# Kernel optimization log

Hardware: AMD Instinct MI355X
Metric: run time of the kernel (lower is better)

Reference implementation:

```python
import jax, jax.numpy as jnp
import numpy as np

EMBED = 2048
HEADS = 16
DFF = 4 * EMBED
EPS = 1e-5


def layernorm(x, g, b):
    mu = jnp.mean(x, axis=-1, keepdims=True)
    var = jnp.var(x, axis=-1, keepdims=True)
    return (x - mu) * jax.lax.rsqrt(var + EPS) * g + b


def setup_inputs() -> dict:
    key = jax.random.key(0)
    ks = jax.random.split(key, 16)
    s = 1.0 / np.sqrt(EMBED)
    sf = 1.0 / np.sqrt(DFF)
    return {
        "x": jax.random.normal(ks[0], (2, 2048, EMBED), jnp.float32),
        "Wq": jax.random.normal(ks[1], (EMBED, EMBED), jnp.float32) * s,
        "bq": jnp.zeros((EMBED,), jnp.float32),
        "Wk": jax.random.normal(ks[2], (EMBED, EMBED), jnp.float32) * s,
        "bk": jnp.zeros((EMBED,), jnp.float32),
        "Wv": jax.random.normal(ks[3], (EMBED, EMBED), jnp.float32) * s,
        "bv": jnp.zeros((EMBED,), jnp.float32),
        "Wo": jax.random.normal(ks[4], (EMBED, EMBED), jnp.float32) * s,
        "bo": jnp.zeros((EMBED,), jnp.float32),
        "g1": jnp.ones((EMBED,), jnp.float32),
        "b1": jnp.zeros((EMBED,), jnp.float32),
        "g2": jnp.ones((EMBED,), jnp.float32),
        "b2": jnp.zeros((EMBED,), jnp.float32),
        "W1": jax.random.normal(ks[5], (EMBED, DFF), jnp.float32) * s,
        "bf1": jnp.zeros((DFF,), jnp.float32),
        "W2": jax.random.normal(ks[6], (DFF, EMBED), jnp.float32) * sf,
        "bf2": jnp.zeros((EMBED,), jnp.float32),
    }


def reference(x, Wq, bq, Wk, bk, Wv, bv, Wo, bo, g1, b1, g2, b2, W1, bf1, W2, bf2):
    B, N, C = x.shape
    H = HEADS
    hd = C // H
    # QKV projections -> [B, H, N, hd]
    def split_heads(t):
        return t.reshape(B, N, H, hd).transpose(0, 2, 1, 3)
    q = split_heads(x @ Wq + bq)
    k = split_heads(x @ Wk + bk)
    v = split_heads(x @ Wv + bv)
    # scores [B, H, N, N]
    attn = jnp.einsum('bhqd,bhkd->bhqk', q, k) / np.sqrt(hd)
    attn = jax.nn.softmax(attn, axis=-1)
    out = jnp.einsum('bhqk,bhkd->bhqd', attn, v)
    out = out.transpose(0, 2, 1, 3).reshape(B, N, C)
    out = out @ Wo + bo
    h = layernorm(x + out, g1, b1)
    ff = jax.nn.gelu(h @ W1 + bf1, approximate=False) @ W2 + bf2
    return layernorm(h + ff, g2, b2)
```

## Files before the change

### kernel.cpp

```cpp
#include <hip/hip_runtime.h>
#include <math.h>

#define EMBED 2048
#define DFF   8192
#define TOK   4096
#define SEQ   2048
#define HEADS 16
#define HD    128
#define LDQ   6144

typedef __attribute__((ext_vector_type(8))) short short8;
typedef __attribute__((ext_vector_type(4))) float f32x4;

__device__ __forceinline__ unsigned short f2bf(float f) {
    unsigned int u = __float_as_uint(f);
    return (unsigned short)((u + 0x7FFFu + ((u >> 16) & 1u)) >> 16);
}
__device__ __forceinline__ float bf2f(unsigned short s) {
    return __uint_as_float(((unsigned int)s) << 16);
}

__device__ __forceinline__ void async16(const void* g, void* l) {
    __builtin_amdgcn_global_load_lds((const __attribute__((address_space(1))) void*)g,
                                     (__attribute__((address_space(3))) void*)l, 16, 0, 0);
}

template<int MODE>
__global__ __launch_bounds__(256, 2)
void gemm_bf16(const unsigned short* __restrict__ A, const unsigned short* __restrict__ B,
               const float* __restrict__ bias, const void* __restrict__ resid,
               unsigned short* __restrict__ C, int M, int N, int K, int lda)
{
    __shared__ unsigned short As[128*32];
    __shared__ unsigned short Bs[128*32];
    const int t = threadIdx.x;
    const int w = t >> 6, l = t & 63;
    const int quad = l >> 4, m16 = l & 15;
    const long bm = (long)blockIdx.y * 128, bn = (long)blockIdx.x * 128;
    const int wr = (w >> 1)*64, wc = (w & 1)*64;

    f32x4 acc[4][4] = {};

    const int srow = w*16 + (l >> 2);
    const int sslot = l & 3;

    for (int k0 = 0; k0 < K; k0 += 32) {
        __syncthreads();
#pragma unroll
        for (int u = 0; u < 2; ++u) {
            const int row = u*64 + srow;
            const int c = sslot ^ ((row >> 1) & 3);
            async16(A + (size_t)(bm + row)*lda + k0 + c*8, As + u*2048 + w*512);
            async16(B + (size_t)(bn + row)*K   + k0 + c*8, Bs + u*2048 + w*512);
        }
        __syncthreads();
        short8 af[4], bf[4];
#pragma unroll
        for (int s = 0; s < 4; ++s) {
            const int ra = wr + s*16 + m16;
            const int sla = quad ^ ((ra >> 1) & 3);
            af[s] = *(const short8*)&As[ra*32 + sla*8];
            const int rb = wc + s*16 + m16;
            const int slb = quad ^ ((rb >> 1) & 3);
            bf[s] = *(const short8*)&Bs[rb*32 + slb*8];
        }
#pragma unroll
        for (int ms = 0; ms < 4; ++ms)
#pragma unroll
            for (int ns = 0; ns < 4; ++ns)
                acc[ms][ns] = __builtin_amdgcn_mfma_f32_16x16x32_bf16(af[ms], bf[ns], acc[ms][ns], 0, 0, 0);
    }

#pragma unroll
    for (int ns = 0; ns < 4; ++ns) {
        const long gc = bn + wc + ns*16 + m16;
        const float bcol = bias[gc];
#pragma unroll
        for (int ms = 0; ms < 4; ++ms) {
#pragma unroll
            for (int r = 0; r < 4; ++r) {
                const long gr = bm + wr + ms*16 + quad*4 + r;
                float v = acc[ms][ns][r] + bcol;
                if (MODE == 1) v += ((const float*)resid)[gr*N + gc];
                if (MODE == 3) v += bf2f(((const unsigned short*)resid)[gr*N + gc]);
                if (MODE == 2) v = 0.5f*v*(1.0f + erff(v*0.70710678118654752f));
                C[gr*N + gc] = f2bf(v);
            }
        }
    }
}

__global__ __launch_bounds__(256, 2)
void attn_flash(unsigned short* __restrict__ qkv)
{
    __shared__ unsigned short Qs[64*128];
    __shared__ unsigned short Ks[64*128];
    __shared__ unsigned short Vt[128*72];
    __shared__ unsigned short Ps[4*16*72];

    const int t = threadIdx.x;
    const int w = t >> 6, l = t & 63;
    const int quad = l >> 4, m16 = l & 15;

    const int qt = blockIdx.x & 31;
    const int bh = blockIdx.x >> 5;
    const int b = bh >> 4, h = bh & 15;

    const long rowq = (long)b*SEQ + qt*64;
    const int qc = h*HD;
    const int kc = EMBED + h*HD;
    const int vc = 2*EMBED + h*HD;

    {
        const int rbase = w*4 + (l >> 4);
        const int slot = l & 15;
#pragma unroll
        for (int u = 0; u < 4; ++u) {
            const int row = u*16 + rbase;
            const int c = slot ^ ((row >> 1) & 7);
            async16(qkv + (rowq + row)*LDQ + qc + c*8, Qs + u*2048 + w*512);
        }
    }
    __syncthreads();

    short8 af[4];
#pragma unroll
    for (int ks = 0; ks < 4; ++ks) {
        const int row = w*16 + m16;
        const int sl = (4*ks + quad) ^ ((row >> 1) & 7);
        af[ks] = *(const short8*)&Qs[row*128 + sl*8];
    }

    f32x4 O[8] = {};
    float mrun[4] = {-1e30f,-1e30f,-1e30f,-1e30f};
    float lrun[4] = {0.f,0.f,0.f,0.f};
    unsigned short* Pw = Ps + w*16*72;

    for (int kt = 0; kt < SEQ/64; ++kt) {
        const long rowkv = (long)b*SEQ + kt*64;
        __syncthreads();
        {
            const int rbase = w*4 + (l >> 4);
            const int slot = l & 15;
#pragma unroll
            for (int u = 0; u < 4; ++u) {
                const int row = u*16 + rbase;
                const int c = slot ^ ((row >> 1) & 7);
                async16(qkv + (rowkv + row)*LDQ + kc + c*8, Ks + u*2048 + w*512);
            }
        }
        {
            const int slot = t & 15;
#pragma unroll
            for (int u = 0; u < 2; ++u) {
                const int rp = u*16 + (t >> 4);
                const short8 va = *(const short8*)(qkv + (rowkv + 2*rp    )*LDQ + vc + slot*8);
                const short8 vb = *(const short8*)(qkv + (rowkv + 2*rp + 1)*LDQ + vc + slot*8);
#pragma unroll
                for (int i = 0; i < 8; ++i) {
                    const int d = slot*8 + i;
                    const int col = (2*rp) ^ (((d >> 5) & 3) << 3);
                    unsigned int pv = (unsigned int)(unsigned short)va[i] |
                                      ((unsigned int)(unsigned short)vb[i] << 16);
                    *(unsigned int*)&Vt[d*72 + col] = pv;
                }
            }
        }
        __syncthreads();

        f32x4 S[4];
#pragma unroll
        for (int ns = 0; ns < 4; ++ns) {
            f32x4 a = {0.f,0.f,0.f,0.f};
            const int row = ns*16 + m16;
            const int swr = (row >> 1) & 7;
#pragma unroll
            for (int ks = 0; ks < 4; ++ks) {
                const int sl = (4*ks + quad) ^ swr;
                const short8 bf = *(const short8*)&Ks[row*128 + sl*8];
                a = __builtin_amdgcn_mfma_f32_16x16x32_bf16(af[ks], bf, a, 0, 0, 0);
            }
#pragma unroll
            for (int r = 0; r < 4; ++r) a[r] *= 0.08838834764831845f;
            S[ns] = a;
        }

        float al[4], rs[4];
#pragma unroll
        for (int r = 0; r < 4; ++r) {
            float tm = fmaxf(fmaxf(S[0][r], S[1][r]), fmaxf(S[2][r], S[3][r]));
            tm = fmaxf(tm, __shfl_xor(tm, 1));
            tm = fmaxf(tm, __shfl_xor(tm, 2));
            tm = fmaxf(tm, __shfl_xor(tm, 4));
            tm = fmaxf(tm, __shfl_xor(tm, 8));
            const float mn = fmaxf(mrun[r], tm);
            al[r] = __expf(mrun[r] - mn);
            mrun[r] = mn;
            rs[r] = 0.f;
        }
#pragma unroll
        for (int ns = 0; ns < 4; ++ns)
#pragma unroll
            for (int r = 0; r < 4; ++r) {
                const float p = __expf(S[ns][r] - mrun[r]);
                rs[r] += p;
                Pw[(quad*4 + r)*72 + ns*16 + m16] = f2bf(p);
            }
#pragma unroll
        for (int r = 0; r < 4; ++r) {
            rs[r] += __shfl_xor(rs[r], 1);
            rs[r] += __shfl_xor(rs[r], 2);
            rs[r] += __shfl_xor(rs[r], 4);
            rs[r] += __shfl_xor(rs[r], 8);
            lrun[r] = lrun[r]*al[r] + rs[r];
        }
#pragma unroll
        for (int i = 0; i < 8; ++i)
#pragma unroll
            for (int r = 0; r < 4; ++r) O[i][r] *= al[r];

#pragma unroll
        for (int ks2 = 0; ks2 < 2; ++ks2) {
            const short8 ap = *(const short8*)&Pw[m16*72 + ks2*32 + quad*8];
#pragma unroll
            for (int ds = 0; ds < 8; ++ds) {
                const int d = ds*16 + m16;
                const int jcol = (ks2*32 + quad*8) ^ (((d >> 5) & 3) << 3);
                const short8 bv = *(const short8*)&Vt[d*72 + jcol];
                O[ds] = __builtin_amdgcn_mfma_f32_16x16x32_bf16(ap, bv, O[ds], 0, 0, 0);
            }
        }
    }

    float inv[4];
#pragma unroll
    for (int r = 0; r < 4; ++r) inv[r] = 1.0f / lrun[r];
#pragma unroll
    for (int ds = 0; ds < 8; ++ds)
#pragma unroll
        for (int r = 0; r < 4; ++r) {
            const long row = rowq + w*16 + quad*4 + r;
            qkv[row*LDQ + qc + ds*16 + m16] = f2bf(O[ds][r] * inv[r]);
        }
}

template<int OUTF32>
__global__ __launch_bounds__(256)
void ln_bf16(const unsigned short* __restrict__ X, const float* __restrict__ g,
             const float* __restrict__ be, void* __restrict__ Y)
{
    __shared__ float r1[256], r2[256];
    const int t = threadIdx.x;
    const long row = blockIdx.x;
    const unsigned short* x = X + row*EMBED;
    float v[8];
    const short8 xv = *(const short8*)(x + t*8);
    float s = 0.f, s2 = 0.f;
#pragma unroll
    for (int i = 0; i < 8; ++i) {
        v[i] = bf2f((unsigned short)xv[i]);
        s += v[i]; s2 += v[i]*v[i];
    }
    r1[t] = s; r2[t] = s2;
    __syncthreads();
    for (int k = 128; k > 0; k >>= 1) {
        if (t < k) { r1[t] += r1[t+k]; r2[t] += r2[t+k]; }
        __syncthreads();
    }
    const float mu = r1[0] * (1.0f/EMBED);
    const float var = r2[0] * (1.0f/EMBED) - mu*mu;
    const float rstd = rsqrtf(var + 1e-5f);
    if (OUTF32) {
        float* y = (float*)Y + row*EMBED + t*8;
#pragma unroll
        for (int i = 0; i < 8; ++i) y[i] = (v[i]-mu)*rstd*g[t*8+i] + be[t*8+i];
    } else {
        unsigned short* y = (unsigned short*)Y + row*EMBED;
        short8 o;
#pragma unroll
        for (int i = 0; i < 8; ++i) o[i] = (short)f2bf((v[i]-mu)*rstd*g[t*8+i] + be[t*8+i]);
        *(short8*)(y + t*8) = o;
    }
}

__global__ __launch_bounds__(256)
void cvt_transpose(const float* __restrict__ W, unsigned short* __restrict__ Wt, int K, int N)
{
    __shared__ unsigned short T[32][33];
    const int t = threadIdx.x;
    const long n0 = (long)blockIdx.x*32, k0 = (long)blockIdx.y*32;
    {
        const int r = t >> 3, c = (t & 7)*4;
        const float4 vv = *(const float4*)&W[(k0 + r)*N + n0 + c];
        T[r][c+0] = f2bf(vv.x); T[r][c+1] = f2bf(vv.y);
        T[r][c+2] = f2bf(vv.z); T[r][c+3] = f2bf(vv.w);
    }
    __syncthreads();
    const int rn = t >> 3, kk = (t & 7)*4;
    unsigned int p0 = (unsigned int)T[kk+0][rn] | ((unsigned int)T[kk+1][rn] << 16);
    unsigned int p1 = (unsigned int)T[kk+2][rn] | ((unsigned int)T[kk+3][rn] << 16);
    unsigned int* dst = (unsigned int*)&Wt[(n0 + rn)*K + k0 + kk];
    dst[0] = p0; dst[1] = p1;
}

__global__ __launch_bounds__(256)
void cvt_f32_bf16(const float* __restrict__ X, unsigned short* __restrict__ Y, long n)
{
    const long i = ((long)blockIdx.x*256 + threadIdx.x)*8;
    if (i >= n) return;
    const float4 a = *(const float4*)&X[i];
    const float4 b = *(const float4*)&X[i+4];
    short8 o;
    o[0]=(short)f2bf(a.x); o[1]=(short)f2bf(a.y); o[2]=(short)f2bf(a.z); o[3]=(short)f2bf(a.w);
    o[4]=(short)f2bf(b.x); o[5]=(short)f2bf(b.y); o[6]=(short)f2bf(b.z); o[7]=(short)f2bf(b.w);
    *(short8*)&Y[i] = o;
}

__global__ __launch_bounds__(256)
void concat_bias(const float* __restrict__ bq, const float* __restrict__ bk,
                 const float* __restrict__ bv, float* __restrict__ out)
{
    const int i = blockIdx.x*256 + threadIdx.x;
    if (i < 2048) out[i] = bq[i];
    else if (i < 4096) out[i] = bk[i-2048];
    else if (i < 6144) out[i] = bv[i-4096];
}

extern "C" void kernel_launch(void* const* d_in, const int* in_sizes, int n_in,
                              void* d_out, int out_size, void* d_ws, size_t ws_size,
                              hipStream_t stream)
{
    const float* x   = (const float*)d_in[0];
    const float* Wq  = (const float*)d_in[1];
    const float* bq  = (const float*)d_in[2];
    const float* Wk  = (const float*)d_in[3];
    const float* bk  = (const float*)d_in[4];
    const float* Wv  = (const float*)d_in[5];
    const float* bv  = (const float*)d_in[6];
    const float* Wo  = (const float*)d_in[7];
    const float* bo  = (const float*)d_in[8];
    const float* g1  = (const float*)d_in[9];
    const float* b1  = (const float*)d_in[10];
    const float* g2v = (const float*)d_in[11];
    const float* b2v = (const float*)d_in[12];
    const float* W1  = (const float*)d_in[13];
    const float* bf1 = (const float*)d_in[14];
    const float* W2  = (const float*)d_in[15];
    const float* bf2 = (const float*)d_in[16];
    float* out = (float*)d_out;

    char* ws = (char*)d_ws;
    unsigned short* Wqkvt = (unsigned short*)(ws + 0);
    unsigned short* Wot   = (unsigned short*)(ws + 25165824);
    unsigned short* W1t   = (unsigned short*)(ws + 33554432);
    unsigned short* W2t   = (unsigned short*)(ws + 67108864);
    float*          bqkv  = (float*)         (ws + 100663296);
    char* arenaA = ws + 100687872;
    unsigned short* xb   = (unsigned short*)(arenaA);
    unsigned short* qkv  = (unsigned short*)(arenaA + 16777216);
    unsigned short* res1 = (unsigned short*)(arenaA);
    unsigned short* ff   = (unsigned short*)(arenaA);
    unsigned short* hb   = (unsigned short*)(ws + 167796736);
    unsigned short* res2 = (unsigned short*)(ws + 0);

    const dim3 blk(256);

    cvt_transpose<<<dim3(64,64),  blk, 0, stream>>>(Wq, Wqkvt,             2048, 2048);
    cvt_transpose<<<dim3(64,64),  blk, 0, stream>>>(Wk, Wqkvt + 2048*2048, 2048, 2048);
    cvt_transpose<<<dim3(64,64),  blk, 0, stream>>>(Wv, Wqkvt + 2*2048*2048, 2048, 2048);
    cvt_transpose<<<dim3(64,64),  blk, 0, stream>>>(Wo, Wot, 2048, 2048);
    cvt_transpose<<<dim3(256,64), blk, 0, stream>>>(W1, W1t, 2048, 8192);
    cvt_transpose<<<dim3(64,256), blk, 0, stream>>>(W2, W2t, 8192, 2048);
    concat_bias<<<dim3(24), blk, 0, stream>>>(bq, bk, bv, bqkv);
    cvt_f32_bf16<<<dim3(4096), blk, 0, stream>>>(x, xb, (long)TOK*EMBED);

    gemm_bf16<0><<<dim3(48,32), blk, 0, stream>>>(xb, Wqkvt, bqkv, nullptr, qkv, TOK, 6144, 2048, 2048);
    attn_flash<<<dim3(1024), blk, 0, stream>>>(qkv);
    gemm_bf16<1><<<dim3(16,32), blk, 0, stream>>>(qkv, Wot, bo, x, res1, TOK, 2048, 2048, 6144);
    ln_bf16<0><<<dim3(4096), blk, 0, stream>>>(res1, g1, b1, hb);
    gemm_bf16<2><<<dim3(64,32), blk, 0, stream>>>(hb, W1t, bf1, nullptr, ff, TOK, 8192, 2048, 2048);
    gemm_bf16<3><<<dim3(16,32), blk, 0, stream>>>(ff, W2t, bf2, hb, res2, TOK, 2048, 8192, 8192);
    ln_bf16<1><<<dim3(4096), blk, 0, stream>>>(res2, g2v, b2v, out);
}
```

Baseline: 1.014 ms.

## Double-buffer LDS tiles in GEMM and flash attention, swizzle GEMM block order

The GEMM kernel now uses two LDS buffers per operand. It issues the async global-to-LDS loads for the next K slice before the MFMAs on the current slice, which removes one barrier per iteration and overlaps memory with compute. The attention kernel double-buffers the K and transposed-V tiles: next-tile K is loaded asynchronously and next-tile V is held in registers, then written transposed after the PV MFMAs. Q shares storage with the second V buffer to save LDS. GEMM launches become 1D with a remap that interleaves block IDs in groups of 8 to change L2/XCD locality. The cost is more LDS per block, which could limit occupancy, and higher register pressure in attention.

```diff
diff --git a/kernel.cpp b/kernel.cpp
--- a/kernel.cpp
+++ b/kernel.cpp
@@ -31,38 +31,57 @@
                const float* __restrict__ bias, const void* __restrict__ resid,
                unsigned short* __restrict__ C, int M, int N, int K, int lda)
 {
-    __shared__ unsigned short As[128*32];
-    __shared__ unsigned short Bs[128*32];
+    __shared__ unsigned short As[2][128*32];
+    __shared__ unsigned short Bs[2][128*32];
     const int t = threadIdx.x;
     const int w = t >> 6, l = t & 63;
     const int quad = l >> 4, m16 = l & 15;
-    const long bm = (long)blockIdx.y * 128, bn = (long)blockIdx.x * 128;
+
+    const int chunk = gridDim.x >> 3;
+    const int lin = (blockIdx.x & 7) * chunk + (blockIdx.x >> 3);
+    const long bm = (long)(lin & 31) * 128;
+    const long bn = (long)(lin >> 5) * 128;
+
     const int wr = (w >> 1)*64, wc = (w & 1)*64;
-
     f32x4 acc[4][4] = {};
 
     const int srow = w*16 + (l >> 2);
     const int sslot = l & 3;
-
-    for (int k0 = 0; k0 < K; k0 += 32) {
+    const unsigned short* Ag = A + (size_t)bm*lda;
+    const unsigned short* Bg = B + (size_t)bn*K;
+
+#pragma unroll
+    for (int u = 0; u < 2; ++u) {
+        const int row = u*64 + srow;
+        const int c = sslot ^ ((row >> 1) & 3);
+        async16(Ag + (size_t)row*lda + c*8, &As[0][u*2048 + w*512]);
+        async16(Bg + (size_t)row*K   + c*8, &Bs[0][u*2048 + w*512]);
+    }
+
+    const int iters = K >> 5;
+    for (int it = 0; it < iters; ++it) {
         __syncthreads();
-#pragma unroll
-        for (int u = 0; u < 2; ++u) {
-            const int row = u*64 + srow;
-            const int c = sslot ^ ((row >> 1) & 3);
-            async16(A + (size_t)(bm + row)*lda + k0 + c*8, As + u*2048 + w*512);
-            async16(B + (size_t)(bn + row)*K   + k0 + c*8, Bs + u*2048 + w*512);
-        }
-        __syncthreads();
+        if (it + 1 < iters) {
+            const int k0 = (it + 1) << 5;
+            const int bsel = (it + 1) & 1;
+#pragma unroll
+            for (int u = 0; u < 2; ++u) {
+                const int row = u*64 + srow;
+                const int c = sslot ^ ((row >> 1) & 3);
+                async16(Ag + (size_t)row*lda + k0 + c*8, &As[bsel][u*2048 + w*512]);
+                async16(Bg + (size_t)row*K   + k0 + c*8, &Bs[bsel][u*2048 + w*512]);
+            }
+        }
+        const int cs = it & 1;
         short8 af[4], bf[4];
 #pragma unroll
         for (int s = 0; s < 4; ++s) {
             const int ra = wr + s*16 + m16;
             const int sla = quad ^ ((ra >> 1) & 3);
-            af[s] = *(const short8*)&As[ra*32 + sla*8];
+            af[s] = *(const short8*)&As[cs][ra*32 + sla*8];
             const int rb = wc + s*16 + m16;
             const int slb = quad ^ ((rb >> 1) & 3);
-            bf[s] = *(const short8*)&Bs[rb*32 + slb*8];
+            bf[s] = *(const short8*)&Bs[cs][rb*32 + slb*8];
         }
 #pragma unroll
         for (int ms = 0; ms < 4; ++ms)
@@ -93,10 +112,10 @@
 __global__ __launch_bounds__(256, 2)
 void attn_flash(unsigned short* __restrict__ qkv)
 {
-    __shared__ unsigned short Qs[64*128];
-    __shared__ unsigned short Ks[64*128];
-    __shared__ unsigned short Vt[128*72];
+    __shared__ unsigned short Ks[2][64*128];
+    __shared__ unsigned short Vt[2][128*72];
     __shared__ unsigned short Ps[4*16*72];
+    unsigned short* Qs = &Vt[1][0];
 
     const int t = threadIdx.x;
     const int w = t >> 6, l = t & 63;
@@ -111,15 +130,31 @@
     const int kc = EMBED + h*HD;
     const int vc = 2*EMBED + h*HD;
 
-    {
-        const int rbase = w*4 + (l >> 4);
-        const int slot = l & 15;
-#pragma unroll
-        for (int u = 0; u < 4; ++u) {
-            const int row = u*16 + rbase;
-            const int c = slot ^ ((row >> 1) & 7);
-            async16(qkv + (rowq + row)*LDQ + qc + c*8, Qs + u*2048 + w*512);
-        }
+    const int rbase = w*4 + (l >> 4);
+    const int slot16 = l & 15;
+    const int vslot = t & 15;
+    const int vrow = t >> 4;
+
+    const int NT = SEQ / 64;
+
+#pragma unroll
+    for (int u = 0; u < 4; ++u) {
+        const int row = u*16 + rbase;
+        const int c = slot16 ^ ((row >> 1) & 7);
+        async16(qkv + (rowq + row)*LDQ + qc + c*8, Qs + u*2048 + w*512);
+    }
+#pragma unroll
+    for (int u = 0; u < 4; ++u) {
+        const int row = u*16 + rbase;
+        const int c = slot16 ^ ((row >> 1) & 7);
+        async16(qkv + ((long)b*SEQ + row)*LDQ + kc + c*8, &Ks[0][u*2048 + w*512]);
+    }
+    short8 va[2], vb[2];
+#pragma unroll
+    for (int u = 0; u < 2; ++u) {
+        const int rp = u*16 + vrow;
+        va[u] = *(const short8*)(qkv + ((long)b*SEQ + 2*rp    )*LDQ + vc + vslot*8);
+        vb[u] = *(const short8*)(qkv + ((long)b*SEQ + 2*rp + 1)*LDQ + vc + vslot*8);
     }
     __syncthreads();
 
@@ -130,43 +165,44 @@
         const int sl = (4*ks + quad) ^ ((row >> 1) & 7);
         af[ks] = *(const short8*)&Qs[row*128 + sl*8];
     }
+#pragma unroll
+    for (int u = 0; u < 2; ++u) {
+        const int rp = u*16 + vrow;
+#pragma unroll
+        for (int i = 0; i < 8; ++i) {
+            const int d = vslot*8 + i;
+            const int col = (2*rp) ^ (((d >> 5) & 3) << 3);
+            unsigned int pv = (unsigned int)(unsigned short)va[u][i] |
+                              ((unsigned int)(unsigned short)vb[u][i] << 16);
+            *(unsigned int*)&Vt[0][d*72 + col] = pv;
+        }
+    }
+    __syncthreads();
 
     f32x4 O[8] = {};
     float mrun[4] = {-1e30f,-1e30f,-1e30f,-1e30f};
     float lrun[4] = {0.f,0.f,0.f,0.f};
     unsigned short* Pw = Ps + w*16*72;
 
-    for (int kt = 0; kt < SEQ/64; ++kt) {
-        const long rowkv = (long)b*SEQ + kt*64;
-        __syncthreads();
-        {
-            const int rbase = w*4 + (l >> 4);
-            const int slot = l & 15;
+    for (int kt = 0; kt < NT; ++kt) {
+        if (kt > 0) __syncthreads();
+        if (kt + 1 < NT) {
+            const long rownext = (long)b*SEQ + (kt + 1)*64;
+            const int bsel = (kt + 1) & 1;
 #pragma unroll
             for (int u = 0; u < 4; ++u) {
                 const int row = u*16 + rbase;
-                const int c = slot ^ ((row >> 1) & 7);
-                async16(qkv + (rowkv + row)*LDQ + kc + c*8, Ks + u*2048 + w*512);
-            }
-        }
-        {
-            const int slot = t & 15;
+                const int c = slot16 ^ ((row >> 1) & 7);
+                async16(qkv + (rownext + row)*LDQ + kc + c*8, &Ks[bsel][u*2048 + w*512]);
+            }
 #pragma unroll
             for (int u = 0; u < 2; ++u) {
-                const int rp = u*16 + (t >> 4);
-                const short8 va = *(const short8*)(qkv + (rowkv + 2*rp    )*LDQ + vc + slot*8);
-                const short8 vb = *(const short8*)(qkv + (rowkv + 2*rp + 1)*LDQ + vc + slot*8);
-#pragma unroll
-                for (int i = 0; i < 8; ++i) {
-                    const int d = slot*8 + i;
-                    const int col = (2*rp) ^ (((d >> 5) & 3) << 3);
-                    unsigned int pv = (unsigned int)(unsigned short)va[i] |
-                                      ((unsigned int)(unsigned short)vb[i] << 16);
-                    *(unsigned int*)&Vt[d*72 + col] = pv;
-                }
-            }
-        }
-        __syncthreads();
+                const int rp = u*16 + vrow;
+                va[u] = *(const short8*)(qkv + (rownext + 2*rp    )*LDQ + vc + vslot*8);
+                vb[u] = *(const short8*)(qkv + (rownext + 2*rp + 1)*LDQ + vc + vslot*8);
+            }
+        }
+        const int cs = kt & 1;
 
         f32x4 S[4];
 #pragma unroll
@@ -177,8 +213,8 @@
 #pragma unroll
             for (int ks = 0; ks < 4; ++ks) {
                 const int sl = (4*ks + quad) ^ swr;
-                const short8 bf = *(const short8*)&Ks[row*128 + sl*8];
-                a = __builtin_amdgcn_mfma_f32_16x16x32_bf16(af[ks], bf, a, 0, 0, 0);
+                const short8 bfr = *(const short8*)&Ks[cs][row*128 + sl*8];
+                a = __builtin_amdgcn_mfma_f32_16x16x32_bf16(af[ks], bfr, a, 0, 0, 0);
             }
 #pragma unroll
             for (int r = 0; r < 4; ++r) a[r] *= 0.08838834764831845f;
@@ -226,8 +262,24 @@
             for (int ds = 0; ds < 8; ++ds) {
                 const int d = ds*16 + m16;
                 const int jcol = (ks2*32 + quad*8) ^ (((d >> 5) & 3) << 3);
-                const short8 bv = *(const short8*)&Vt[d*72 + jcol];
+                const short8 bv = *(const short8*)&Vt[cs][d*72 + jcol];
                 O[ds] = __builtin_amdgcn_mfma_f32_16x16x32_bf16(ap, bv, O[ds], 0, 0, 0);
+            }
+        }
+
+        if (kt + 1 < NT) {
+            const int bsel = (kt + 1) & 1;
+#pragma unroll
+            for (int u = 0; u < 2; ++u) {
+                const int rp = u*16 + vrow;
+#pragma unroll
+                for (int i = 0; i < 8; ++i) {
+                    const int d = vslot*8 + i;
+                    const int col = (2*rp) ^ (((d >> 5) & 3) << 3);
+                    unsigned int pv = (unsigned int)(unsigned short)va[u][i] |
+                                      ((unsigned int)(unsigned short)vb[u][i] << 16);
+                    *(unsigned int*)&Vt[bsel][d*72 + col] = pv;
+                }
             }
         }
     }
@@ -374,11 +426,11 @@
     concat_bias<<<dim3(24), blk, 0, stream>>>(bq, bk, bv, bqkv);
     cvt_f32_bf16<<<dim3(4096), blk, 0, stream>>>(x, xb, (long)TOK*EMBED);
 
-    gemm_bf16<0><<<dim3(48,32), blk, 0, stream>>>(xb, Wqkvt, bqkv, nullptr, qkv, TOK, 6144, 2048, 2048);
+    gemm_bf16<0><<<dim3(32*48), blk, 0, stream>>>(xb, Wqkvt, bqkv, nullptr, qkv, TOK, 6144, 2048, 2048);
     attn_flash<<<dim3(1024), blk, 0, stream>>>(qkv);
-    gemm_bf16<1><<<dim3(16,32), blk, 0, stream>>>(qkv, Wot, bo, x, res1, TOK, 2048, 2048, 6144);
+    gemm_bf16<1><<<dim3(32*16), blk, 0, stream>>>(qkv, Wot, bo, x, res1, TOK, 2048, 2048, 6144);
     ln_bf16<0><<<dim3(4096), blk, 0, stream>>>(res1, g1, b1, hb);
-    gemm_bf16<2><<<dim3(64,32), blk, 0, stream>>>(hb, W1t, bf1, nullptr, ff, TOK, 8192, 2048, 2048);
-    gemm_bf16<3><<<dim3(16,32), blk, 0, stream>>>(ff, W2t, bf2, hb, res2, TOK, 2048, 8192, 8192);
+    gemm_bf16<2><<<dim3(32*64), blk, 0, stream>>>(hb, W1t, bf1, nullptr, ff, TOK, 8192, 2048, 2048);
+    gemm_bf16<3><<<dim3(32*16), blk, 0, stream>>>(ff, W2t, bf2, hb, res2, TOK, 2048, 8192, 8192);
     ln_bf16<1><<<dim3(4096), blk, 0, stream>>>(res2, g2v, b2v, out);
 }
```

Result: slower. 1.063 ms (+4.8%).

## Double-buffer GEMM LDS tiles, stage epilogue through LDS, use tanh GELU

Applied to the files above, without the earlier changes.

The GEMM main loop now double-buffers the A/B tiles in LDS. The global-to-LDS loads for the next K-step are issued before computing the current one, which leaves one barrier per iteration instead of two. The epilogue stages accumulators through LDS so each thread writes 8 contiguous bf16 outputs and reads the residual with vector loads, replacing scattered 2-byte stores. The erf-based GELU is replaced by the tanh/sigmoid approximation using __expf. This trades a small numerical deviation from the exact GELU for cheaper arithmetic.

```diff
diff --git a/kernel.cpp b/kernel.cpp
--- a/kernel.cpp
+++ b/kernel.cpp
@@ -25,14 +25,22 @@
                                      (__attribute__((address_space(3))) void*)l, 16, 0, 0);
 }
 
+__device__ __forceinline__ float gelu_fast(float v) {
+    const float y = 1.5957691216057308f * (v + 0.044715f * v * v * v);
+    return v / (1.0f + __expf(-y));
+}
+
 template<int MODE>
 __global__ __launch_bounds__(256, 2)
 void gemm_bf16(const unsigned short* __restrict__ A, const unsigned short* __restrict__ B,
                const float* __restrict__ bias, const void* __restrict__ resid,
                unsigned short* __restrict__ C, int M, int N, int K, int lda)
 {
-    __shared__ unsigned short As[128*32];
-    __shared__ unsigned short Bs[128*32];
+    __shared__ __align__(16) float smemf[8448];
+    unsigned short* As = (unsigned short*)smemf;
+    unsigned short* Bs = As + 8192;
+    float* Cs = smemf;
+
     const int t = threadIdx.x;
     const int w = t >> 6, l = t & 63;
     const int quad = l >> 4, m16 = l & 15;
@@ -43,26 +51,41 @@
 
     const int srow = w*16 + (l >> 2);
     const int sslot = l & 3;
-
-    for (int k0 = 0; k0 < K; k0 += 32) {
-        __syncthreads();
-#pragma unroll
-        for (int u = 0; u < 2; ++u) {
-            const int row = u*64 + srow;
-            const int c = sslot ^ ((row >> 1) & 3);
-            async16(A + (size_t)(bm + row)*lda + k0 + c*8, As + u*2048 + w*512);
-            async16(B + (size_t)(bn + row)*K   + k0 + c*8, Bs + u*2048 + w*512);
-        }
-        __syncthreads();
+    const unsigned short* Ag = A + (size_t)bm*lda;
+    const unsigned short* Bg = B + (size_t)bn*K;
+
+#pragma unroll
+    for (int u = 0; u < 2; ++u) {
+        const int row = u*64 + srow;
+        const int c = sslot ^ ((row >> 1) & 3);
+        async16(Ag + (size_t)row*lda + c*8, &As[u*2048 + w*512]);
+        async16(Bg + (size_t)row*K   + c*8, &Bs[u*2048 + w*512]);
+    }
+
+    const int iters = K >> 5;
+    for (int it = 0; it < iters; ++it) {
+        __syncthreads();
+        if (it + 1 < iters) {
+            const int k0 = (it + 1) << 5;
+            const int bo = ((it + 1) & 1) * 4096;
+#pragma unroll
+            for (int u = 0; u < 2; ++u) {
+                const int row = u*64 + srow;
+                const int c = sslot ^ ((row >> 1) & 3);
+                async16(Ag + (size_t)row*lda + k0 + c*8, &As[bo + u*2048 + w*512]);
+                async16(Bg + (size_t)row*K   + k0 + c*8, &Bs[bo + u*2048 + w*512]);
+            }
+        }
+        const int co = (it & 1) * 4096;
         short8 af[4], bf[4];
 #pragma unroll
         for (int s = 0; s < 4; ++s) {
             const int ra = wr + s*16 + m16;
             const int sla = quad ^ ((ra >> 1) & 3);
-            af[s] = *(const short8*)&As[ra*32 + sla*8];
+            af[s] = *(const short8*)&As[co + ra*32 + sla*8];
             const int rb = wc + s*16 + m16;
             const int slb = quad ^ ((rb >> 1) & 3);
-            bf[s] = *(const short8*)&Bs[rb*32 + slb*8];
+            bf[s] = *(const short8*)&Bs[co + rb*32 + slb*8];
         }
 #pragma unroll
         for (int ms = 0; ms < 4; ++ms)
@@ -71,21 +94,49 @@
                 acc[ms][ns] = __builtin_amdgcn_mfma_f32_16x16x32_bf16(af[ms], bf[ns], acc[ms][ns], 0, 0, 0);
     }
 
-#pragma unroll
-    for (int ns = 0; ns < 4; ++ns) {
-        const long gc = bn + wc + ns*16 + m16;
-        const float bcol = bias[gc];
-#pragma unroll
-        for (int ms = 0; ms < 4; ++ms) {
-#pragma unroll
-            for (int r = 0; r < 4; ++r) {
-                const long gr = bm + wr + ms*16 + quad*4 + r;
-                float v = acc[ms][ns][r] + bcol;
-                if (MODE == 1) v += ((const float*)resid)[gr*N + gc];
-                if (MODE == 3) v += bf2f(((const unsigned short*)resid)[gr*N + gc]);
-                if (MODE == 2) v = 0.5f*v*(1.0f + erff(v*0.70710678118654752f));
-                C[gr*N + gc] = f2bf(v);
-            }
+    const int ecol = (t & 15) * 8;
+    float bias8[8];
+#pragma unroll
+    for (int i = 0; i < 8; ++i) bias8[i] = bias[bn + ecol + i];
+
+#pragma unroll
+    for (int pass = 0; pass < 2; ++pass) {
+        __syncthreads();
+        if ((w >> 1) == pass) {
+#pragma unroll
+            for (int ms = 0; ms < 4; ++ms)
+#pragma unroll
+                for (int ns = 0; ns < 4; ++ns)
+#pragma unroll
+                    for (int r = 0; r < 4; ++r)
+                        Cs[(ms*16 + quad*4 + r)*132 + wc + ns*16 + m16] = acc[ms][ns][r];
+        }
+        __syncthreads();
+#pragma unroll
+        for (int j = 0; j < 4; ++j) {
+            const int row = j*16 + (t >> 4);
+            float v[8];
+            *(f32x4*)&v[0] = *(const f32x4*)&Cs[row*132 + ecol];
+            *(f32x4*)&v[4] = *(const f32x4*)&Cs[row*132 + ecol + 4];
+            const long gr = bm + pass*64 + row;
+            const long go = gr*N + bn + ecol;
+            float r8[8];
+            if (MODE == 1) {
+                *(f32x4*)&r8[0] = *(const f32x4*)((const float*)resid + go);
+                *(f32x4*)&r8[4] = *(const f32x4*)((const float*)resid + go + 4);
+            }
+            short8 rb16;
+            if (MODE == 3) rb16 = *(const short8*)((const unsigned short*)resid + go);
+            short8 o;
+#pragma unroll
+            for (int i = 0; i < 8; ++i) {
+                float y = v[i] + bias8[i];
+                if (MODE == 1) y += r8[i];
+                if (MODE == 3) y += bf2f((unsigned short)rb16[i]);
+                if (MODE == 2) y = gelu_fast(y);
+                o[i] = (short)f2bf(y);
+            }
+            *(short8*)&C[go] = o;
         }
     }
 }
@@ -146,7 +197,7 @@
             for (int u = 0; u < 4; ++u) {
                 const int row = u*16 + rbase;
                 const int c = slot ^ ((row >> 1) & 7);
-                async16(qkv + (rowkv + row)*LDQ + kc + c*8, Ks + u*2048 + w*512);
+                async16(qkv + (rowkv + row)*LDQ + kc + c*8, &Ks[u*2048 + w*512]);
             }
         }
         {
@@ -177,8 +228,8 @@
 #pragma unroll
             for (int ks = 0; ks < 4; ++ks) {
                 const int sl = (4*ks + quad) ^ swr;
-                const short8 bf = *(const short8*)&Ks[row*128 + sl*8];
-                a = __builtin_amdgcn_mfma_f32_16x16x32_bf16(af[ks], bf, a, 0, 0, 0);
+                const short8 bfr = *(const short8*)&Ks[row*128 + sl*8];
+                a = __builtin_amdgcn_mfma_f32_16x16x32_bf16(af[ks], bfr, a, 0, 0, 0);
             }
 #pragma unroll
             for (int r = 0; r < 4; ++r) a[r] *= 0.08838834764831845f;
```

After: 951.4 us. 6.2% less time.
